# Kernel optimization log

Hardware: AMD Instinct MI355X
Metric: run time of the kernel (lower is better)

## Reference

```python
import jax, jax.numpy as jnp
import numpy as np

N = 8192          # num_points
RADIUS = 0.5


def _make_curve(num_points):
    # Reproduces the interp1d-based turbo-coil curve from __init__ (linear interp).
    xk = np.array([-2, -1, 0, 1, 1, 0, -1, -1, 0, 1, 2], dtype=np.float64)
    zk = np.array([0, 0, 1, 0, -1, 0, 1, 0, -1, 0, 0], dtype=np.float64)
    yk = np.array([0, 0, 1, 1, -1, -1, -1, 1, 1, 0, 0], dtype=np.float64)
    t = np.linspace(0.0, 1.0, len(xk))
    s = np.linspace(0.0, 1.0, num_points)
    return (np.interp(s, t, xk).astype(np.float32),
            np.interp(s, t, yk).astype(np.float32),
            np.interp(s, t, zk).astype(np.float32))


def setup_inputs() -> dict:
    x, y, z = _make_curve(N)
    return {"x": jnp.asarray(x), "y": jnp.asarray(y), "z": jnp.asarray(z)}


def _cdist(a, b):
    # pairwise Euclidean distance, safe at zero (subgradient 0 like torch.cdist)
    d2 = jnp.sum(a * a, -1, keepdims=True) - 2.0 * (a @ b.T) + jnp.sum(b * b, -1)
    d2 = jnp.maximum(d2, 0.0)
    safe = jnp.where(d2 > 0.0, d2, 1.0)
    return jnp.where(d2 > 0.0, jnp.sqrt(safe), 0.0)


def _mask_distances(dist, min_dist):
    # Original: for each row i, scan j = i, i+1, ... and overwrite entries with
    # min_dist+1 while dist[i,j] <= min_dist, breaking at the first entry that
    # exceeds min_dist (the j in range(i,0) loop is empty, so only the forward
    # scan matters). Vectorized: contiguous prefix-run starting at the diagonal.
    n = dist.shape[0]
    rows = jnp.arange(n)[:, None]
    cols = jnp.arange(n)[None, :]
    upper = cols >= rows
    cond = dist <= min_dist
    # cumprod along each row, seeded with 1 (True) left of the diagonal, so that
    # run[i,j] = all(cond[i, i..j]) for j >= i
    run = jnp.cumprod(jnp.where(upper, cond, True).astype(jnp.int32), axis=1)
    mask = upper & (run > 0)
    return jnp.where(mask, min_dist + 1.0, dist)


def _puffer_loss(p2d, low, high):
    # PufferZone(points_2d, -1.0, 1.0, x): out-of-bounds penalty on [low, high]
    return jax.nn.relu(p2d - high) + jax.nn.relu(low - p2d)


def _noise_loss(p2d):
    # noise_reduction_loss: penalize curvature (squared second differences)
    d2 = p2d[2:] - 2.0 * p2d[1:-1] + p2d[:-2]
    return d2 * d2


def reference(x, y, z, scale=1.0):
    p2d = jnp.stack([y, z], axis=1)          # [N, 2]
    p3d = jnp.stack([x, y, z], axis=1)       # [N, 3]

    fixed = _puffer_loss(p2d, -1.0, 1.0)

    dist = _cdist(p3d, p3d)                  # [N, N]
    min_dist = RADIUS * 2.0 * scale
    dist_mask = _mask_distances(dist, min_dist)
    intersect = jax.nn.relu(min_dist - dist_mask)

    noise = _noise_loss(p2d)

    # dist_loss (WeightedEuclideanDistance) taken as the pairwise cdist sum
    return (jnp.sum(fixed)
            + jnp.sum(dist) / 10000.0
            + jnp.sum(intersect)
            + jnp.sum(noise) * 10.0)
```

## Files before the change

### kernel.cpp

```cpp
#include <hip/hip_runtime.h>

constexpr int N = 8192;
constexpr float TRI = 33558528.0f;

__device__ __forceinline__ float fsqrt(float v) { return __builtin_amdgcn_sqrtf(v); }

__global__ __launch_bounds__(256, 4)
void main_kernel(const float* __restrict__ x, const float* __restrict__ y,
                 const float* __restrict__ z,
                 float* __restrict__ row_sd, float* __restrict__ row_sm,
                 float* __restrict__ row_corr) {
    const int tid  = threadIdx.x;
    const int lane = tid & 63;
    const int wave = tid >> 6;
    __shared__ float lsd[4][8];
    __shared__ float lsm[4][8];

    if (blockIdx.x < 1024) {
        const int b       = blockIdx.x;
        const int topBase = 4 * b;
        const int botBase = N - 4 * (b + 1);

        float xr[8], yr[8], zr[8];
#pragma unroll
        for (int r = 0; r < 4; ++r) {
            xr[r]     = x[topBase + r]; yr[r]     = y[topBase + r]; zr[r]     = z[topBase + r];
            xr[4 + r] = x[botBase + r]; yr[4 + r] = y[botBase + r]; zr[4 + r] = z[botBase + r];
        }
        float sd[8], sm[8];
#pragma unroll
        for (int r = 0; r < 8; ++r) { sd[r] = 0.f; sm[r] = 0.f; }

#pragma unroll
        for (int g = 0; g < 2; ++g) {
            const int base = g ? botBase : topBase;
            const int ro   = g * 4;

            {
                const int   j  = base + tid;
                const int   jc = (j < N) ? j : (N - 1);
                const float cx = x[jc], cy = y[jc], cz = z[jc];
#pragma unroll
                for (int r = 0; r < 4; ++r) {
                    const float dx = cx - xr[ro + r], dy = cy - yr[ro + r], dz = cz - zr[ro + r];
                    const float d  = fsqrt(dx * dx + dy * dy + dz * dz);
                    if (tid >= r && j < N) { sd[ro + r] += d; sm[ro + r] += fminf(d, 1.f); }
                }
            }
            int j0 = base + 256;
            if (j0 + 256 <= N) {
                float nx = x[j0 + tid], ny = y[j0 + tid], nz = z[j0 + tid];
                while (true) {
                    const float cx = nx, cy = ny, cz = nz;
                    const bool  more = (j0 + 512 <= N);
                    if (more) {
                        const int jn = j0 + 256 + tid;
                        nx = x[jn]; ny = y[jn]; nz = z[jn];
                    }
#pragma unroll
                    for (int r = 0; r < 4; ++r) {
                        const float dx = cx - xr[ro + r], dy = cy - yr[ro + r], dz = cz - zr[ro + r];
                        const float d  = fsqrt(dx * dx + dy * dy + dz * dz);
                        sd[ro + r] += d; sm[ro + r] += fminf(d, 1.f);
                    }
                    j0 += 256;
                    if (!more) break;
                }
            }
            if (j0 < N) {
                const int j = j0 + tid;
                if (j < N) {
                    const float cx = x[j], cy = y[j], cz = z[j];
#pragma unroll
                    for (int r = 0; r < 4; ++r) {
                        const float dx = cx - xr[ro + r], dy = cy - yr[ro + r], dz = cz - zr[ro + r];
                        const float d  = fsqrt(dx * dx + dy * dy + dz * dz);
                        sd[ro + r] += d; sm[ro + r] += fminf(d, 1.f);
                    }
                }
            }
        }

#pragma unroll
        for (int r = 0; r < 8; ++r) {
            float a = sd[r], c = sm[r];
#pragma unroll
            for (int off = 32; off; off >>= 1) {
                a += __shfl_down(a, off);
                c += __shfl_down(c, off);
            }
            if (lane == 0) { lsd[wave][r] = a; lsm[wave][r] = c; }
        }
        __syncthreads();
        if (tid < 8) {
            const float a = lsd[0][tid] + lsd[1][tid] + lsd[2][tid] + lsd[3][tid];
            const float c = lsm[0][tid] + lsm[1][tid] + lsm[2][tid] + lsm[3][tid];
            const int   i = (tid < 4) ? (topBase + tid) : (botBase + tid - 4);
            row_sd[i] = a;
            row_sm[i] = c;
        }
    } else {
        const int cb = blockIdx.x - 1024;
#pragma unroll
        for (int rr = 0; rr < 2; ++rr) {
            const int   i  = 8 * cb + 2 * wave + rr;
            const float xi = x[i], yi = y[i], zi = z[i];
            float corr = 0.f;
            for (int jb = i; jb < N; jb += 64) {
                const int j = jb + lane;
                float d = 2.f;
                if (j < N) {
                    const float dx = x[j] - xi, dy = y[j] - yi, dz = z[j] - zi;
                    d = fsqrt(dx * dx + dy * dy + dz * dz);
                }
                const unsigned long long far = __ballot(d > 1.0f);
                const int stop = far ? __builtin_ctzll(far) : 64;
                if (lane < stop) corr += 1.f - d;
                if (far) break;
            }
#pragma unroll
            for (int off = 32; off; off >>= 1) corr += __shfl_down(corr, off);
            if (lane == 0) row_corr[i] = corr;
        }
    }
}

__global__ __launch_bounds__(256)
void finalize_kernel(const float* __restrict__ y, const float* __restrict__ z,
                     const float* __restrict__ row_sd, const float* __restrict__ row_sm,
                     const float* __restrict__ row_corr, float* __restrict__ out) {
    const int tid = threadIdx.x;
    float A = 0.f, M = 0.f, C = 0.f, sfix = 0.f, snoise = 0.f;
    for (int i = tid; i < N; i += 256) {
        A += row_sd[i];
        M += row_sm[i];
        C += row_corr[i];
        const float yv = y[i], zv = z[i];
        sfix += fmaxf(yv - 1.f, 0.f) + fmaxf(-1.f - yv, 0.f)
              + fmaxf(zv - 1.f, 0.f) + fmaxf(-1.f - zv, 0.f);
        if (i < N - 2) {
            const float d2y = y[i + 2] - 2.f * y[i + 1] + y[i];
            const float d2z = z[i + 2] - 2.f * z[i + 1] + z[i];
            snoise += d2y * d2y + d2z * d2z;
        }
    }
    __shared__ float s[5][256];
    s[0][tid] = A; s[1][tid] = M; s[2][tid] = C; s[3][tid] = sfix; s[4][tid] = snoise;
    __syncthreads();
    for (int st = 128; st; st >>= 1) {
        if (tid < st) {
#pragma unroll
            for (int k = 0; k < 5; ++k) s[k][tid] += s[k][tid + st];
        }
        __syncthreads();
    }
    if (tid == 0)
        out[0] = s[3][0] + (2.f * s[0][0]) / 10000.f
               + (2.f * (TRI - s[1][0]) - (float)N - s[2][0]) + 10.f * s[4][0];
}

extern "C" void kernel_launch(void* const* d_in, const int* in_sizes, int n_in,
                              void* d_out, int out_size, void* d_ws, size_t ws_size,
                              hipStream_t stream) {
    const float* x = (const float*)d_in[0];
    const float* y = (const float*)d_in[1];
    const float* z = (const float*)d_in[2];
    float* out      = (float*)d_out;
    float* row_sd   = (float*)d_ws;
    float* row_sm   = row_sd + N;
    float* row_corr = row_sm + N;

    main_kernel<<<2048, 256, 0, stream>>>(x, y, z, row_sd, row_sm, row_corr);
    finalize_kernel<<<1, 256, 0, stream>>>(y, z, row_sd, row_sm, row_corr, out);
}
```

Before: 35.32 us.

## Pack points into float4 layout, prefetch correction scan, split final reduction

A new pack kernel interleaves x, y, z into a float4 array so that the main kernel does one 16-byte load per point instead of three scalar loads. The correction-scan branch now handles 128 columns per iteration and prefetches the next chunk. Launch bounds are raised to 8 blocks per CU. The single-block finalize is split into a 32-block partial reduction plus a tiny final kernel. Together these add two extra kernel launches and a workspace write of the packed points, which may cancel the load savings on this small problem.

Measured after the change: 29.26 us. 17.2% less time.

```diff
diff --git a/kernel.cpp b/kernel.cpp
--- a/kernel.cpp
+++ b/kernel.cpp
@@ -5,16 +5,21 @@
 
 __device__ __forceinline__ float fsqrt(float v) { return __builtin_amdgcn_sqrtf(v); }
 
-__global__ __launch_bounds__(256, 4)
-void main_kernel(const float* __restrict__ x, const float* __restrict__ y,
-                 const float* __restrict__ z,
+
+__global__ __launch_bounds__(256)
+void pack_kernel(const float* __restrict__ x, const float* __restrict__ y,
+                 const float* __restrict__ z, float4* __restrict__ p4) {
+    const int i = blockIdx.x * 256 + threadIdx.x;
+    p4[i] = make_float4(x[i], y[i], z[i], 0.f);
+}
+
+__global__ __launch_bounds__(256, 8)
+void main_kernel(const float4* __restrict__ p4,
                  float* __restrict__ row_sd, float* __restrict__ row_sm,
                  float* __restrict__ row_corr) {
     const int tid  = threadIdx.x;
     const int lane = tid & 63;
     const int wave = tid >> 6;
-    __shared__ float lsd[4][8];
-    __shared__ float lsm[4][8];
 
     if (blockIdx.x < 1024) {
         const int b       = blockIdx.x;
@@ -24,8 +29,10 @@
         float xr[8], yr[8], zr[8];
 #pragma unroll
         for (int r = 0; r < 4; ++r) {
-            xr[r]     = x[topBase + r]; yr[r]     = y[topBase + r]; zr[r]     = z[topBase + r];
-            xr[4 + r] = x[botBase + r]; yr[4 + r] = y[botBase + r]; zr[4 + r] = z[botBase + r];
+            const float4 pt = p4[topBase + r];
+            const float4 pb = p4[botBase + r];
+            xr[r]     = pt.x; yr[r]     = pt.y; zr[r]     = pt.z;
+            xr[4 + r] = pb.x; yr[4 + r] = pb.y; zr[4 + r] = pb.z;
         }
         float sd[8], sm[8];
 #pragma unroll
@@ -37,29 +44,26 @@
             const int ro   = g * 4;
 
             {
-                const int   j  = base + tid;
-                const int   jc = (j < N) ? j : (N - 1);
-                const float cx = x[jc], cy = y[jc], cz = z[jc];
+                const int    j  = base + tid;
+                const int    jc = (j < N) ? j : (N - 1);
+                const float4 p  = p4[jc];
 #pragma unroll
                 for (int r = 0; r < 4; ++r) {
-                    const float dx = cx - xr[ro + r], dy = cy - yr[ro + r], dz = cz - zr[ro + r];
+                    const float dx = p.x - xr[ro + r], dy = p.y - yr[ro + r], dz = p.z - zr[ro + r];
                     const float d  = fsqrt(dx * dx + dy * dy + dz * dz);
-                    if (tid >= r && j < N) { sd[ro + r] += d; sm[ro + r] += fminf(d, 1.f); }
+                    if (j < N && tid >= r) { sd[ro + r] += d; sm[ro + r] += fminf(d, 1.f); }
                 }
             }
             int j0 = base + 256;
             if (j0 + 256 <= N) {
-                float nx = x[j0 + tid], ny = y[j0 + tid], nz = z[j0 + tid];
+                float4 p = p4[j0 + tid];
                 while (true) {
-                    const float cx = nx, cy = ny, cz = nz;
-                    const bool  more = (j0 + 512 <= N);
-                    if (more) {
-                        const int jn = j0 + 256 + tid;
-                        nx = x[jn]; ny = y[jn]; nz = z[jn];
-                    }
+                    const float4 c    = p;
+                    const bool   more = (j0 + 512 <= N);
+                    if (more) p = p4[j0 + 256 + tid];
 #pragma unroll
                     for (int r = 0; r < 4; ++r) {
-                        const float dx = cx - xr[ro + r], dy = cy - yr[ro + r], dz = cz - zr[ro + r];
+                        const float dx = c.x - xr[ro + r], dy = c.y - yr[ro + r], dz = c.z - zr[ro + r];
                         const float d  = fsqrt(dx * dx + dy * dy + dz * dz);
                         sd[ro + r] += d; sm[ro + r] += fminf(d, 1.f);
                     }
@@ -70,10 +74,10 @@
             if (j0 < N) {
                 const int j = j0 + tid;
                 if (j < N) {
-                    const float cx = x[j], cy = y[j], cz = z[j];
+                    const float4 p = p4[j];
 #pragma unroll
                     for (int r = 0; r < 4; ++r) {
-                        const float dx = cx - xr[ro + r], dy = cy - yr[ro + r], dz = cz - zr[ro + r];
+                        const float dx = p.x - xr[ro + r], dy = p.y - yr[ro + r], dz = p.z - zr[ro + r];
                         const float d  = fsqrt(dx * dx + dy * dy + dz * dz);
                         sd[ro + r] += d; sm[ro + r] += fminf(d, 1.f);
                     }
@@ -81,6 +85,8 @@
             }
         }
 
+        __shared__ float lsd[4][8];
+        __shared__ float lsm[4][8];
 #pragma unroll
         for (int r = 0; r < 8; ++r) {
             float a = sd[r], c = sm[r];
@@ -103,20 +109,31 @@
         const int cb = blockIdx.x - 1024;
 #pragma unroll
         for (int rr = 0; rr < 2; ++rr) {
-            const int   i  = 8 * cb + 2 * wave + rr;
-            const float xi = x[i], yi = y[i], zi = z[i];
+            const int    i  = 8 * cb + 2 * wave + rr;
+            const float4 pi = p4[i];
             float corr = 0.f;
-            for (int jb = i; jb < N; jb += 64) {
-                const int j = jb + lane;
-                float d = 2.f;
-                if (j < N) {
-                    const float dx = x[j] - xi, dy = y[j] - yi, dz = z[j] - zi;
-                    d = fsqrt(dx * dx + dy * dy + dz * dz);
-                }
-                const unsigned long long far = __ballot(d > 1.0f);
-                const int stop = far ? __builtin_ctzll(far) : 64;
-                if (lane < stop) corr += 1.f - d;
-                if (far) break;
+            int   jb   = i;
+            float4 a  = p4[min(jb + lane,      N - 1)];
+            float4 bq = p4[min(jb + 64 + lane, N - 1)];
+            while (true) {
+                const float4 na = p4[min(jb + 128 + lane, N - 1)];
+                const float4 nb = p4[min(jb + 192 + lane, N - 1)];
+                const int j0i = jb + lane, j1i = jb + 64 + lane;
+                float dx = a.x - pi.x, dy = a.y - pi.y, dz = a.z - pi.z;
+                const float d0 = fsqrt(dx * dx + dy * dy + dz * dz);
+                dx = bq.x - pi.x; dy = bq.y - pi.y; dz = bq.z - pi.z;
+                const float d1 = fsqrt(dx * dx + dy * dy + dz * dz);
+                const unsigned long long m0 = __ballot(j0i >= N || d0 > 1.f);
+                const unsigned long long m1 = __ballot(j1i >= N || d1 > 1.f);
+                int stop;
+                if (m0)      stop = __builtin_ctzll(m0);
+                else if (m1) stop = 64 + __builtin_ctzll(m1);
+                else         stop = 128;
+                if (lane < stop)      corr += 1.f - d0;
+                if (64 + lane < stop) corr += 1.f - d1;
+                if (stop < 128) break;
+                jb += 128;
+                a = na; bq = nb;
             }
 #pragma unroll
             for (int off = 32; off; off >>= 1) corr += __shfl_down(corr, off);
@@ -126,37 +143,59 @@
 }
 
 __global__ __launch_bounds__(256)
-void finalize_kernel(const float* __restrict__ y, const float* __restrict__ z,
-                     const float* __restrict__ row_sd, const float* __restrict__ row_sm,
-                     const float* __restrict__ row_corr, float* __restrict__ out) {
+void partial_kernel(const float* __restrict__ y, const float* __restrict__ z,
+                    const float* __restrict__ row_sd, const float* __restrict__ row_sm,
+                    const float* __restrict__ row_corr, float* __restrict__ partials) {
     const int tid = threadIdx.x;
-    float A = 0.f, M = 0.f, C = 0.f, sfix = 0.f, snoise = 0.f;
-    for (int i = tid; i < N; i += 256) {
-        A += row_sd[i];
-        M += row_sm[i];
-        C += row_corr[i];
-        const float yv = y[i], zv = z[i];
-        sfix += fmaxf(yv - 1.f, 0.f) + fmaxf(-1.f - yv, 0.f)
-              + fmaxf(zv - 1.f, 0.f) + fmaxf(-1.f - zv, 0.f);
-        if (i < N - 2) {
-            const float d2y = y[i + 2] - 2.f * y[i + 1] + y[i];
-            const float d2z = z[i + 2] - 2.f * z[i + 1] + z[i];
-            snoise += d2y * d2y + d2z * d2z;
-        }
-    }
-    __shared__ float s[5][256];
-    s[0][tid] = A; s[1][tid] = M; s[2][tid] = C; s[3][tid] = sfix; s[4][tid] = snoise;
+    const int i   = blockIdx.x * 256 + tid;
+    float v[5];
+    v[0] = row_sd[i];
+    v[1] = row_sm[i];
+    v[2] = row_corr[i];
+    const float yv = y[i], zv = z[i];
+    v[3] = fmaxf(yv - 1.f, 0.f) + fmaxf(-1.f - yv, 0.f)
+         + fmaxf(zv - 1.f, 0.f) + fmaxf(-1.f - zv, 0.f);
+    v[4] = 0.f;
+    if (i < N - 2) {
+        const float d2y = y[i + 2] - 2.f * y[i + 1] + y[i];
+        const float d2z = z[i + 2] - 2.f * z[i + 1] + z[i];
+        v[4] = d2y * d2y + d2z * d2z;
+    }
+    const int lane = tid & 63, wave = tid >> 6;
+    __shared__ float s[4][5];
+#pragma unroll
+    for (int c = 0; c < 5; ++c) {
+        float a = v[c];
+#pragma unroll
+        for (int off = 32; off; off >>= 1) a += __shfl_down(a, off);
+        if (lane == 0) s[wave][c] = a;
+    }
     __syncthreads();
-    for (int st = 128; st; st >>= 1) {
-        if (tid < st) {
-#pragma unroll
-            for (int k = 0; k < 5; ++k) s[k][tid] += s[k][tid + st];
-        }
-        __syncthreads();
-    }
-    if (tid == 0)
-        out[0] = s[3][0] + (2.f * s[0][0]) / 10000.f
-               + (2.f * (TRI - s[1][0]) - (float)N - s[2][0]) + 10.f * s[4][0];
+    if (tid == 0) {
+#pragma unroll
+        for (int c = 0; c < 5; ++c)
+            partials[blockIdx.x * 5 + c] = s[0][c] + s[1][c] + s[2][c] + s[3][c];
+    }
+}
+
+__global__ __launch_bounds__(64)
+void final_kernel(const float* __restrict__ partials, float* __restrict__ out) {
+    const int tid = threadIdx.x;
+    float a[5] = {0.f, 0.f, 0.f, 0.f, 0.f};
+    if (tid < 32) {
+#pragma unroll
+        for (int c = 0; c < 5; ++c) a[c] = partials[tid * 5 + c];
+    }
+#pragma unroll
+    for (int c = 0; c < 5; ++c) {
+#pragma unroll
+        for (int off = 16; off; off >>= 1) a[c] += __shfl_down(a[c], off, 32);
+    }
+    if (tid == 0) {
+        const float A = a[0], M = a[1], C = a[2], fix = a[3], noise = a[4];
+        out[0] = fix + (2.f * A) / 10000.f
+               + (2.f * (TRI - M) - (float)N - C) + 10.f * noise;
+    }
 }
 
 extern "C" void kernel_launch(void* const* d_in, const int* in_sizes, int n_in,
@@ -166,10 +205,14 @@
     const float* y = (const float*)d_in[1];
     const float* z = (const float*)d_in[2];
     float* out      = (float*)d_out;
-    float* row_sd   = (float*)d_ws;
+    float4* p4      = (float4*)d_ws;
+    float* row_sd   = (float*)(p4 + N);
     float* row_sm   = row_sd + N;
     float* row_corr = row_sm + N;
-
-    main_kernel<<<2048, 256, 0, stream>>>(x, y, z, row_sd, row_sm, row_corr);
-    finalize_kernel<<<1, 256, 0, stream>>>(y, z, row_sd, row_sm, row_corr, out);
-}
+    float* partials = row_corr + N;
+
+    pack_kernel<<<N / 256, 256, 0, stream>>>(x, y, z, p4);
+    main_kernel<<<2048, 256, 0, stream>>>(p4, row_sd, row_sm, row_corr);
+    partial_kernel<<<32, 256, 0, stream>>>(y, z, row_sd, row_sm, row_corr, partials);
+    final_kernel<<<1, 64, 0, stream>>>(partials, out);
+}
```
